# Kernel optimization log

Measured on AMD Instinct MI355X. Metric: run time of the kernel, lower is better.

## Reference

```python
import jax, jax.numpy as jnp
import numpy as np

B, S, H, NH = 4, 2048, 1024, 16
HD = H // NH  # 64


def setup_inputs() -> dict:
    key = jax.random.key(0)
    ks = jax.random.split(key, 9)
    s = 1.0 / np.sqrt(H)
    return {
        "hidden_state": jax.random.normal(ks[0], (B, S, H), dtype=jnp.float32),
        "Wq": jax.random.normal(ks[1], (H, H), dtype=jnp.float32) * s,
        "bq": jnp.zeros((H,), dtype=jnp.float32),
        "Wk": jax.random.normal(ks[2], (H, HD), dtype=jnp.float32) * s,
        "bk": jnp.zeros((HD,), dtype=jnp.float32),
        "Wv": jax.random.normal(ks[3], (H, HD), dtype=jnp.float32) * s,
        "bv": jnp.zeros((HD,), dtype=jnp.float32),
        "Wo": jax.random.normal(ks[4], (H, H), dtype=jnp.float32) * s,
        "bo": jnp.zeros((H,), dtype=jnp.float32),
    }


def reference(hidden_state, Wq, bq, Wk, bk, Wv, bv, Wo, bo):
    b, s = hidden_state.shape[0], hidden_state.shape[1]
    q = hidden_state @ Wq + bq                      # [B,S,H]
    k = hidden_state @ Wk + bk                      # [B,S,HD] (single shared KV head)
    v = hidden_state @ Wv + bv                      # [B,S,HD]
    q = q.reshape(b, s, NH, HD).transpose(0, 2, 1, 3)  # [B,NH,S,HD]
    scale = 1.0 / jnp.sqrt(jnp.float32(HD))
    # shared K head: broadcast over NH without materializing expanded K/V
    scores = jnp.einsum("bhqd,bkd->bhqk", q, k) * scale  # [B,NH,S,S]
    probs = jax.nn.softmax(scores, axis=-1)
    out = jnp.einsum("bhqk,bkd->bhqd", probs, v)         # [B,NH,S,HD]
    out = out.transpose(0, 2, 1, 3).reshape(b, s, NH * HD)
    return out @ Wo + bo
```

## Files before the change

### kernel.cpp

```cpp
#include <hip/hip_runtime.h>
#include <hip/hip_bf16.h>
#include <stdint.h>

#define B_ 4
#define S_ 2048
#define H_ 1024
#define NH_ 16
#define HD_ 64

typedef __bf16 bf16x8 __attribute__((ext_vector_type(8)));
typedef float floatx4 __attribute__((ext_vector_type(4)));
typedef float floatx16 __attribute__((ext_vector_type(16)));

__device__ __forceinline__ float b2f(unsigned short u) {
  union { float f; unsigned int i; } x; x.i = ((unsigned int)u) << 16; return x.f;
}
__device__ __forceinline__ unsigned short f2b(float f) {
  unsigned int u = __float_as_uint(f);
  u += 0x7fff + ((u >> 16) & 1);
  return (unsigned short)(u >> 16);
}

__device__ __forceinline__ void gload_lds16(const unsigned short* g, unsigned short* l) {
  __builtin_amdgcn_global_load_lds(
      (const __attribute__((address_space(1))) unsigned int*)(uintptr_t)g,
      (__attribute__((address_space(3))) unsigned int*)(uintptr_t)l,
      16, 0, 0);
}


__global__ __launch_bounds__(256) void convert_f32_bf16(
    const float* __restrict__ s, unsigned short* __restrict__ d, int n) {
  int i0 = (blockIdx.x * 256 + threadIdx.x) * 8;
  if (i0 >= n) return;
  float4 a = *(const float4*)(s + i0);
  float4 b = *(const float4*)(s + i0 + 4);
  union { unsigned short u[8]; uint4 v; } p;
  p.u[0] = f2b(a.x); p.u[1] = f2b(a.y); p.u[2] = f2b(a.z); p.u[3] = f2b(a.w);
  p.u[4] = f2b(b.x); p.u[5] = f2b(b.y); p.u[6] = f2b(b.z); p.u[7] = f2b(b.w);
  *(uint4*)(d + i0) = p.v;
}

__global__ __launch_bounds__(256) void transpose_f32_bf16(
    const float* __restrict__ src, unsigned short* __restrict__ dst,
    int R, int C) {
  __shared__ unsigned short tile[64][65];
  const int c0 = blockIdx.x * 64;
  const int r0 = blockIdx.y * 64;
  const int tx = threadIdx.x;
  const int ty = threadIdx.y;
  for (int i = ty; i < 64; i += 4)
    tile[i][tx] = f2b(src[(size_t)(r0 + i) * C + c0 + tx]);
  __syncthreads();
  for (int i = ty; i < 64; i += 4)
    dst[(size_t)(c0 + i) * R + r0 + tx] = tile[tx][i];
}

__global__ void build_kvbias(const float* __restrict__ bk,
                             const float* __restrict__ bv,
                             float* __restrict__ kvb) {
  int i = threadIdx.x;
  kvb[i] = (i < 64) ? bk[i] : bv[i - 64];
}

__global__ __launch_bounds__(256) void kf_build(const unsigned short* __restrict__ KVm,
                                                unsigned short* __restrict__ KF) {
  int tid = blockIdx.x * 256 + threadIdx.x;
  int L = tid & 63, u = tid >> 6;
  int cq = u & 3, kt = (u >> 2) & 1, kb = (u >> 3) & 31, b = u >> 8;
  int row = b * 2048 + kb * 64 + kt * 32 + (L & 31);
  int col = cq * 16 + (L >> 5) * 8;
  *(uint4*)(KF + (size_t)tid * 8) = *(const uint4*)(KVm + (size_t)row * 128 + col);
}

__global__ __launch_bounds__(256) void vf_build(const unsigned short* __restrict__ KVm,
                                                unsigned short* __restrict__ VF) {
  int tid = blockIdx.x * 256 + threadIdx.x;
  int L = tid & 63, u = tid >> 6;
  int dt = u & 1, kh = (u >> 1) & 1, kt = (u >> 2) & 1, kb = (u >> 3) & 31, b = u >> 8;
  int krow0 = b * 2048 + kb * 64 + kt * 32 + kh * 16 + (L >> 5) * 8;
  int d = dt * 32 + (L & 31);
  union { unsigned short t[8]; uint4 v; } tmp;
#pragma unroll
  for (int j = 0; j < 8; j++) tmp.t[j] = KVm[(size_t)(krow0 + j) * 128 + 64 + d];
  *(uint4*)(VF + (size_t)tid * 8) = tmp.v;
}


__global__ __launch_bounds__(256) void gemm_qkv(
    const unsigned short* __restrict__ A,
    const unsigned short* __restrict__ Bt,
    const float* __restrict__ bq,
    const float* __restrict__ kvb,
    unsigned short* __restrict__ Qm,
    unsigned short* __restrict__ KVm,
    int M, int K) {
  __shared__ unsigned short As[4096];
  __shared__ unsigned short Bs[4096];
  const int m0 = blockIdx.x * 128;
  const int n0 = blockIdx.y * 128;
  const int t = threadIdx.x;
  const int lane = t & 63;
  const int w = t >> 6;
  const int wr = (w & 1) * 64;
  const int wc = (w >> 1) * 64;
  const int lrow = lane & 15;
  const int lk = (lane >> 4) * 8;

  floatx4 acc[4][4] = {};

  const unsigned short* Ap = A + (size_t)(m0 + (t >> 2)) * K + (t & 3) * 8;
  const unsigned short* Bp = Bt + (size_t)(n0 + (t >> 2)) * K + (t & 3) * 8;
  const size_t rowstep = (size_t)64 * K;

  for (int k0 = 0; k0 < K; k0 += 32) {
    __syncthreads();
    gload_lds16(Ap + k0,           &As[w * 512]);
    gload_lds16(Ap + k0 + rowstep, &As[2048 + w * 512]);
    gload_lds16(Bp + k0,           &Bs[w * 512]);
    gload_lds16(Bp + k0 + rowstep, &Bs[2048 + w * 512]);
    __syncthreads();
    bf16x8 a[4], b[4];
#pragma unroll
    for (int i = 0; i < 4; i++)
      a[i] = *(const bf16x8*)&As[(wr + i * 16 + lrow) * 32 + lk];
#pragma unroll
    for (int j = 0; j < 4; j++)
      b[j] = *(const bf16x8*)&Bs[(wc + j * 16 + lrow) * 32 + lk];
#pragma unroll
    for (int i = 0; i < 4; i++)
#pragma unroll
      for (int j = 0; j < 4; j++)
        acc[i][j] = __builtin_amdgcn_mfma_f32_16x16x32_bf16(a[i], b[j], acc[i][j], 0, 0, 0);
  }
  const bool isQ = (n0 < 1024);
#pragma unroll
  for (int j = 0; j < 4; j++) {
    int col = n0 + wc + j * 16 + lrow;
    float bj = isQ ? bq[col] : kvb[col - 1024];
#pragma unroll
    for (int i = 0; i < 4; i++) {
      int row0 = m0 + wr + i * 16 + (lane >> 4) * 4;
#pragma unroll
      for (int r = 0; r < 4; r++) {
        unsigned short v = f2b(acc[i][j][r] + bj);
        if (isQ) Qm[(size_t)(row0 + r) * 1024 + col] = v;
        else     KVm[(size_t)(row0 + r) * 128 + col - 1024] = v;
      }
    }
  }
}


__global__ __launch_bounds__(256) void gemm_out(
    const unsigned short* __restrict__ A,
    const unsigned short* __restrict__ Bt,
    const float* __restrict__ bias,
    float* __restrict__ C,
    int M, int N, int K) {
  __shared__ unsigned short As[4096];
  __shared__ unsigned short Bs[4096];
  const int m0 = blockIdx.x * 128;
  const int n0 = blockIdx.y * 128;
  const int t = threadIdx.x;
  const int lane = t & 63;
  const int w = t >> 6;
  const int wr = (w & 1) * 64;
  const int wc = (w >> 1) * 64;
  const int lrow = lane & 15;
  const int lk = (lane >> 4) * 8;

  floatx4 acc[4][4] = {};

  const unsigned short* Ap = A + (size_t)(m0 + (t >> 2)) * K + (t & 3) * 8;
  const unsigned short* Bp = Bt + (size_t)(n0 + (t >> 2)) * K + (t & 3) * 8;
  const size_t rowstep = (size_t)64 * K;

  for (int k0 = 0; k0 < K; k0 += 32) {
    __syncthreads();
    gload_lds16(Ap + k0,           &As[w * 512]);
    gload_lds16(Ap + k0 + rowstep, &As[2048 + w * 512]);
    gload_lds16(Bp + k0,           &Bs[w * 512]);
    gload_lds16(Bp + k0 + rowstep, &Bs[2048 + w * 512]);
    __syncthreads();
    bf16x8 a[4], b[4];
#pragma unroll
    for (int i = 0; i < 4; i++)
      a[i] = *(const bf16x8*)&As[(wr + i * 16 + lrow) * 32 + lk];
#pragma unroll
    for (int j = 0; j < 4; j++)
      b[j] = *(const bf16x8*)&Bs[(wc + j * 16 + lrow) * 32 + lk];
#pragma unroll
    for (int i = 0; i < 4; i++)
#pragma unroll
      for (int j = 0; j < 4; j++)
        acc[i][j] = __builtin_amdgcn_mfma_f32_16x16x32_bf16(a[i], b[j], acc[i][j], 0, 0, 0);
  }
#pragma unroll
  for (int j = 0; j < 4; j++) {
    int col = n0 + wc + j * 16 + lrow;
    float bj = bias[col];
#pragma unroll
    for (int i = 0; i < 4; i++) {
      int row0 = m0 + wr + i * 16 + (lane >> 4) * 4;
#pragma unroll
      for (int r = 0; r < 4; r++)
        C[(size_t)(row0 + r) * N + col] = acc[i][j][r] + bj;
    }
  }
}


__global__ __launch_bounds__(64) void mqa_flash2(
    const unsigned short* __restrict__ Qm,
    const unsigned short* __restrict__ KF,
    const unsigned short* __restrict__ VF,
    unsigned short* __restrict__ O) {
  __shared__ unsigned short T[32 * 72];

  const int bid = blockIdx.x;
  const int q32 = bid & 63;
  const int h = (bid >> 6) & 15;
  const int b = bid >> 10;
  const int L = threadIdx.x;
  const int q = L & 31;
  const int hw = L >> 5;

  const float scale2 = 0.125f * 1.44269504088896340736f;
  const float CAP = 10.0f;

  const int qrow = b * S_ + q32 * 32 + q;
  bf16x8 qf[4];
#pragma unroll
  for (int cq = 0; cq < 4; cq++)
    qf[cq] = *(const bf16x8*)(Qm + (size_t)qrow * 1024 + h * 64 + cq * 16 + hw * 8);

  floatx16 oacc[2] = {};
  float l = 0.f;

  const unsigned short* kfp = KF + (size_t)b * 131072 + L * 8;
  const unsigned short* vfp = VF + (size_t)b * 131072 + L * 8;

  bf16x8 kA[8], kB[8];
#pragma unroll
  for (int u = 0; u < 8; u++) kA[u] = *(const bf16x8*)(kfp + u * 512);

  for (int kb = 0; kb < 32; kb++) {
    bf16x8 vr[8];
    const unsigned short* vp = vfp + (size_t)kb * 4096;
#pragma unroll
    for (int u = 0; u < 8; u++) vr[u] = *(const bf16x8*)(vp + u * 512);

    const bf16x8* kcur = (kb & 1) ? kB : kA;
    bf16x8* knxt = (kb & 1) ? kA : kB;

    floatx16 sacc[2] = {};
#pragma unroll
    for (int kt = 0; kt < 2; kt++)
#pragma unroll
      for (int cq = 0; cq < 4; cq++)
        sacc[kt] = __builtin_amdgcn_mfma_f32_32x32x16_bf16(kcur[kt * 4 + cq], qf[cq], sacc[kt], 0, 0, 0);

    {
      const unsigned short* kp = kfp + (size_t)(kb + 1) * 4096;
#pragma unroll
      for (int u = 0; u < 8; u++) knxt[u] = *(const bf16x8*)(kp + u * 512);
    }

    unsigned int pk[2][8];
#pragma unroll
    for (int kt = 0; kt < 2; kt++)
#pragma unroll
      for (int i2 = 0; i2 < 8; i2++) {
        float p0 = exp2f(fmaf(sacc[kt][2 * i2],     scale2, -CAP));
        float p1 = exp2f(fmaf(sacc[kt][2 * i2 + 1], scale2, -CAP));
        l += p0 + p1;
        union { __bf16 h2[2]; unsigned int u; } pu;
        pu.h2[0] = (__bf16)p0; pu.h2[1] = (__bf16)p1;
        pk[kt][i2] = pu.u;
      }

#pragma unroll
    for (int kt = 0; kt < 2; kt++)
#pragma unroll
      for (int kh = 0; kh < 2; kh++) {
        unsigned int s0 = hw ? pk[kt][kh * 4 + 0] : pk[kt][kh * 4 + 2];
        unsigned int s1 = hw ? pk[kt][kh * 4 + 1] : pk[kt][kh * 4 + 3];
        unsigned int r0 = (unsigned int)__shfl_xor((int)s0, 32, 64);
        unsigned int r1 = (unsigned int)__shfl_xor((int)s1, 32, 64);
        union { unsigned int u[4]; bf16x8 v; } fu;
        if (hw == 0) {
          fu.u[0] = pk[kt][kh * 4 + 0]; fu.u[1] = pk[kt][kh * 4 + 1];
          fu.u[2] = r0;                 fu.u[3] = r1;
        } else {
          fu.u[0] = r0;                 fu.u[1] = r1;
          fu.u[2] = pk[kt][kh * 4 + 2]; fu.u[3] = pk[kt][kh * 4 + 3];
        }
#pragma unroll
        for (int dt = 0; dt < 2; dt++)
          oacc[dt] = __builtin_amdgcn_mfma_f32_32x32x16_bf16(vr[kt * 4 + kh * 2 + dt], fu.v, oacc[dt], 0, 0, 0);
      }
  }

  l += __shfl_xor(l, 32, 64);
  float inv = 1.0f / l;
#pragma unroll
  for (int dt = 0; dt < 2; dt++)
#pragma unroll
    for (int g = 0; g < 4; g++) {
      int d = dt * 32 + g * 8 + hw * 4;
      union { __bf16 h4[4]; uint2 u; } ou;
#pragma unroll
      for (int r = 0; r < 4; r++) ou.h4[r] = (__bf16)(oacc[dt][g * 4 + r] * inv);
      *(uint2*)&T[q * 72 + d] = ou.u;
    }
  asm volatile("" ::: "memory");
  int q2 = L >> 1, dh = (L & 1) * 32;
  const size_t obase = ((size_t)(b * S_ + q32 * 32 + q2)) * 1024 + h * 64 + dh;
#pragma unroll
  for (int c = 0; c < 4; c++) {
    uint4 vv = *(const uint4*)&T[q2 * 72 + dh + c * 8];
    *(uint4*)(O + obase + c * 8) = vv;
  }
}


extern "C" void kernel_launch(void* const* d_in, const int* in_sizes, int n_in,
                              void* d_out, int out_size, void* d_ws, size_t ws_size,
                              hipStream_t stream) {
  const float* X  = (const float*)d_in[0];
  const float* Wq = (const float*)d_in[1];
  const float* bq = (const float*)d_in[2];
  const float* Wk = (const float*)d_in[3];
  const float* bk = (const float*)d_in[4];
  const float* Wv = (const float*)d_in[5];
  const float* bv = (const float*)d_in[6];
  const float* Wo = (const float*)d_in[7];
  const float* bo = (const float*)d_in[8];
  float* out = (float*)d_out;

  if (ws_size < 40108544) return;
  char* wsb = (char*)d_ws;
  unsigned short* Xc    = (unsigned short*)(wsb);
  unsigned short* WqkvT = (unsigned short*)(wsb + 16777216);
  unsigned short* WoT   = (unsigned short*)(wsb + 19136512);
  float*          kvb   = (float*)(wsb + 21233664);
  unsigned short* Qm    = (unsigned short*)(wsb + 21234176);
  unsigned short* KVm   = (unsigned short*)(wsb + 38011392);
  unsigned short* Om    = Xc;
  unsigned short* KF    = WqkvT;
  unsigned short* VF    = WqkvT + (size_t)524288;

  convert_f32_bf16<<<4096, 256, 0, stream>>>(X, Xc, 8192 * 1024);

  dim3 tb(64, 4);
  transpose_f32_bf16<<<dim3(16, 16), tb, 0, stream>>>(Wq, WqkvT, 1024, 1024);
  transpose_f32_bf16<<<dim3(1, 16),  tb, 0, stream>>>(Wk, WqkvT + (size_t)1024 * 1024, 1024, 64);
  transpose_f32_bf16<<<dim3(1, 16),  tb, 0, stream>>>(Wv, WqkvT + (size_t)1088 * 1024, 1024, 64);
  transpose_f32_bf16<<<dim3(16, 16), tb, 0, stream>>>(Wo, WoT, 1024, 1024);
  build_kvbias<<<1, 128, 0, stream>>>(bk, bv, kvb);

  gemm_qkv<<<dim3(64, 9), 256, 0, stream>>>(Xc, WqkvT, bq, kvb, Qm, KVm, 8192, 1024);
  kf_build<<<256, 256, 0, stream>>>(KVm, KF);
  vf_build<<<256, 256, 0, stream>>>(KVm, VF);
  mqa_flash2<<<4096, 64, 0, stream>>>(Qm, KF, VF, Om);
  gemm_out<<<dim3(64, 8), 256, 0, stream>>>(Om, WoT, bo, out, 8192, 1024, 1024);
}
```

Before: 346.6 us.

## Share K/V tiles across four query waves via LDS in flash kernel

The attention kernel now runs 4 waves per block, each handling its own 32-query tile of the same head. Each K/V block is loaded once into shared memory with global_load_lds and read by all four waves, instead of every wave streaming K/V from global memory into registers. This cuts global/L2 traffic for the shared KV head and frees registers. The cost is two block barriers per iteration and the loss of the previous register double-buffering, so the loads are no longer overlapped with compute.

```diff
diff --git a/kernel.cpp b/kernel.cpp
--- a/kernel.cpp
+++ b/kernel.cpp
@@ -211,25 +211,30 @@
 }
 
 
-__global__ __launch_bounds__(64) void mqa_flash2(
+__global__ __launch_bounds__(256) void mqa_flash3(
     const unsigned short* __restrict__ Qm,
     const unsigned short* __restrict__ KF,
     const unsigned short* __restrict__ VF,
     unsigned short* __restrict__ O) {
-  __shared__ unsigned short T[32 * 72];
+  __shared__ unsigned short Sh[9216];
 
   const int bid = blockIdx.x;
-  const int q32 = bid & 63;
-  const int h = (bid >> 6) & 15;
-  const int b = bid >> 10;
-  const int L = threadIdx.x;
+  const int q128 = bid & 15;
+  const int h = (bid >> 4) & 15;
+  const int b = bid >> 8;
+  const int t = threadIdx.x;
+  const int L = t & 63;
+  const int w = t >> 6;
   const int q = L & 31;
   const int hw = L >> 5;
 
   const float scale2 = 0.125f * 1.44269504088896340736f;
   const float CAP = 10.0f;
 
-  const int qrow = b * S_ + q32 * 32 + q;
+  unsigned short* Ksh = Sh;
+  unsigned short* Vsh = Sh + 4096;
+
+  const int qrow = b * S_ + (q128 * 4 + w) * 32 + q;
   bf16x8 qf[4];
 #pragma unroll
   for (int cq = 0; cq < 4; cq++)
@@ -238,34 +243,27 @@
   floatx16 oacc[2] = {};
   float l = 0.f;
 
-  const unsigned short* kfp = KF + (size_t)b * 131072 + L * 8;
-  const unsigned short* vfp = VF + (size_t)b * 131072 + L * 8;
-
-  bf16x8 kA[8], kB[8];
-#pragma unroll
-  for (int u = 0; u < 8; u++) kA[u] = *(const bf16x8*)(kfp + u * 512);
+  const unsigned short* kfb = KF + (size_t)b * 131072 + t * 8;
+  const unsigned short* vfb = VF + (size_t)b * 131072 + t * 8;
 
   for (int kb = 0; kb < 32; kb++) {
-    bf16x8 vr[8];
-    const unsigned short* vp = vfp + (size_t)kb * 4096;
-#pragma unroll
-    for (int u = 0; u < 8; u++) vr[u] = *(const bf16x8*)(vp + u * 512);
-
-    const bf16x8* kcur = (kb & 1) ? kB : kA;
-    bf16x8* knxt = (kb & 1) ? kA : kB;
+    __syncthreads();
+    const unsigned short* ks = kfb + (size_t)kb * 4096;
+    const unsigned short* vs = vfb + (size_t)kb * 4096;
+    gload_lds16(ks,        &Ksh[w * 512]);
+    gload_lds16(ks + 2048, &Ksh[2048 + w * 512]);
+    gload_lds16(vs,        &Vsh[w * 512]);
+    gload_lds16(vs + 2048, &Vsh[2048 + w * 512]);
+    __syncthreads();
 
     floatx16 sacc[2] = {};
 #pragma unroll
     for (int kt = 0; kt < 2; kt++)
 #pragma unroll
-      for (int cq = 0; cq < 4; cq++)
-        sacc[kt] = __builtin_amdgcn_mfma_f32_32x32x16_bf16(kcur[kt * 4 + cq], qf[cq], sacc[kt], 0, 0, 0);
-
-    {
-      const unsigned short* kp = kfp + (size_t)(kb + 1) * 4096;
-#pragma unroll
-      for (int u = 0; u < 8; u++) knxt[u] = *(const bf16x8*)(kp + u * 512);
-    }
+      for (int cq = 0; cq < 4; cq++) {
+        bf16x8 kf = *(const bf16x8*)&Ksh[(kt * 4 + cq) * 512 + L * 8];
+        sacc[kt] = __builtin_amdgcn_mfma_f32_32x32x16_bf16(kf, qf[cq], sacc[kt], 0, 0, 0);
+      }
 
     unsigned int pk[2][8];
 #pragma unroll
@@ -297,13 +295,17 @@
           fu.u[2] = pk[kt][kh * 4 + 2]; fu.u[3] = pk[kt][kh * 4 + 3];
         }
 #pragma unroll
-        for (int dt = 0; dt < 2; dt++)
-          oacc[dt] = __builtin_amdgcn_mfma_f32_32x32x16_bf16(vr[kt * 4 + kh * 2 + dt], fu.v, oacc[dt], 0, 0, 0);
+        for (int dt = 0; dt < 2; dt++) {
+          bf16x8 vf = *(const bf16x8*)&Vsh[(kt * 4 + kh * 2 + dt) * 512 + L * 8];
+          oacc[dt] = __builtin_amdgcn_mfma_f32_32x32x16_bf16(vf, fu.v, oacc[dt], 0, 0, 0);
+        }
       }
   }
 
   l += __shfl_xor(l, 32, 64);
   float inv = 1.0f / l;
+  __syncthreads();
+  unsigned short* T = Sh + w * 2304;
 #pragma unroll
   for (int dt = 0; dt < 2; dt++)
 #pragma unroll
@@ -316,7 +318,7 @@
     }
   asm volatile("" ::: "memory");
   int q2 = L >> 1, dh = (L & 1) * 32;
-  const size_t obase = ((size_t)(b * S_ + q32 * 32 + q2)) * 1024 + h * 64 + dh;
+  const size_t obase = ((size_t)(b * S_ + (q128 * 4 + w) * 32 + q2)) * 1024 + h * 64 + dh;
 #pragma unroll
   for (int c = 0; c < 4; c++) {
     uint4 vv = *(const uint4*)&T[q2 * 72 + dh + c * 8];
@@ -363,6 +365,6 @@
   gemm_qkv<<<dim3(64, 9), 256, 0, stream>>>(Xc, WqkvT, bq, kvb, Qm, KVm, 8192, 1024);
   kf_build<<<256, 256, 0, stream>>>(KVm, KF);
   vf_build<<<256, 256, 0, stream>>>(KVm, VF);
-  mqa_flash2<<<4096, 64, 0, stream>>>(Qm, KF, VF, Om);
+  mqa_flash3<<<1024, 256, 0, stream>>>(Qm, KF, VF, Om);
   gemm_out<<<dim3(64, 8), 256, 0, stream>>>(Om, WoT, bo, out, 8192, 1024, 1024);
 }
```

New measurement: 307.9 us. -11.2%, faster.
